# Kernel tuning notes

Hardware: AMD Instinct MI355X
Metric: run time of the kernel (lower is better)

The kernel has to match this reference:

```python
import jax, jax.numpy as jnp
import numpy as np

DIM = 64
HID = 128
DT_MAX = 0.1
BATCH = 16384


def _lin_init(k, fi, fo):
    kw, kb = jax.random.split(k)
    s = 1.0 / np.sqrt(fi)
    w = jax.random.uniform(kw, (fi, fo), minval=-s, maxval=s, dtype=jnp.float32)
    b = jax.random.uniform(kb, (fo,), minval=-s, maxval=s, dtype=jnp.float32)
    return w, b


def setup_inputs() -> dict:
    key = jax.random.key(0)
    ks = list(jax.random.split(key, 16))
    it = iter(ks)
    inp = {"z": jax.random.normal(next(it), (BATCH, DIM), dtype=jnp.float32)}
    layouts = [
        ("H", [(DIM, HID), (HID, HID), (HID, 1)]),
        ("D", [(DIM, HID), (HID, HID), (HID, 1)]),
        ("J", [(DIM, HID), (HID, DIM * DIM)]),
        ("B", [(DIM, HID), (HID, DIM * DIM)]),
        ("u", [(DIM, HID), (HID, DIM)]),
    ]
    for name, dims in layouts:
        for li, (fi, fo) in enumerate(dims, 1):
            w, b = _lin_init(next(it), fi, fo)
            inp[f"{name}w{li}"] = w
            inp[f"{name}b{li}"] = b
    inp["dt_logit"] = jnp.zeros((), dtype=jnp.float32)
    inp["energy_target"] = jnp.asarray(1.0, dtype=jnp.float32)
    return inp


def _scalar_net(z, w1, b1, w2, b2, w3, b3):
    # Linear->SiLU->Linear->SiLU->Linear, then softplus, squeeze -> [B]
    h = jax.nn.silu(z @ w1 + b1)
    h = jax.nn.silu(h @ w2 + b2)
    return jax.nn.softplus((h @ w3 + b3)[..., 0])


def reference(z, Hw1, Hb1, Hw2, Hb2, Hw3, Hb3,
              Dw1, Db1, Dw2, Db2, Dw3, Db3,
              Jw1, Jb1, Jw2, Jb2, Bw1, Bb1, Bw2, Bb2,
              uw1, ub1, uw2, ub2, dt_logit, energy_target):
    H = _scalar_net(z, Hw1, Hb1, Hw2, Hb2, Hw3, Hb3)  # [B]
    # autograd.grad(H.sum(), z) / grad(D.sum(), z)
    gH = jax.grad(lambda zz: _scalar_net(zz, Hw1, Hb1, Hw2, Hb2, Hw3, Hb3).sum())(z)
    gD = jax.grad(lambda zz: _scalar_net(zz, Dw1, Db1, Dw2, Db2, Dw3, Db3).sum())(z)
    # skew-symmetric J
    A = (jax.nn.silu(z @ Jw1 + Jb1) @ Jw2 + Jb2).reshape(-1, DIM, DIM)
    Jm = A - jnp.swapaxes(A, 1, 2)
    # PSD R = B B^T
    Bm = (jax.nn.silu(z @ Bw1 + Bb1) @ Bw2 + Bb2).reshape(-1, DIM, DIM)
    R = jnp.einsum('bik,bjk->bij', Bm, Bm)
    cons = jnp.einsum('bij,bj->bi', Jm, gH)
    diss = -jnp.einsum('bij,bj->bi', R, gD)
    u = jnp.tanh(z @ uw1 + ub1) @ uw2 + ub2
    pump = (energy_target - H)[:, None] * u
    dt = jax.nn.sigmoid(dt_logit) * DT_MAX
    dz = cons + diss + 0.1 * pump
    return z + dt * dz
```

## Files before the change

kernel.cpp:

```cpp
#include <hip/hip_runtime.h>

#define DIM 64
#define HID 128

typedef __attribute__((ext_vector_type(8))) short short8;
typedef __attribute__((ext_vector_type(4))) float f32x4;
typedef __attribute__((ext_vector_type(2))) float f32x2;
typedef _Float16 h16x8 __attribute__((ext_vector_type(8)));
typedef _Float16 h16x2 __attribute__((ext_vector_type(2)));
typedef unsigned short ushort_t;

#define MFMA(A, B, C) __builtin_amdgcn_mfma_f32_16x16x32_bf16((A), (B), (C), 0, 0, 0)
#define MFMAH(A, B, C) __builtin_amdgcn_mfma_f32_16x16x32_f16((A), (B), (C), 0, 0, 0)
#define GLOAD_LDS(gp, lp) __builtin_amdgcn_global_load_lds( \
    (const __attribute__((address_space(1))) void*)(gp),    \
    (__attribute__((address_space(3))) void*)(lp), 16, 0, 0)

__device__ __forceinline__ float sigm(float x) { return 1.f / (1.f + __expf(-x)); }
__device__ __forceinline__ float siluf(float x) { return x * sigm(x); }
__device__ __forceinline__ float silup(float x) { float s = sigm(x); return s + x * s * (1.f - s); }
__device__ __forceinline__ float softplusf(float x) {
    if (x > 20.f) return x;
    return log1pf(__expf(x));
}
__device__ __forceinline__ ushort_t f2bf(float f) {
    union { float f; unsigned int u; } v; v.f = f;
    unsigned int r = v.u + 0x7fffu + ((v.u >> 16) & 1u);
    return (ushort_t)(r >> 16);
}
__device__ __forceinline__ ushort_t f2h(float f) {
    _Float16 h = (_Float16)f;
    union { _Float16 h; ushort_t u; } v; v.h = h; return v.u;
}
__device__ __forceinline__ _Float16 u2h(ushort_t u) {
    union { ushort_t u; _Float16 h; } v; v.u = u; return v.h;
}

#define OFF_HW1F  0
#define OFF_HW2F  8192
#define OFF_HW2TF 24576
#define OFF_HW1TF 40960
#define OFF_DW1F  49152
#define OFF_DW2F  57344
#define OFF_DW2TF 73728
#define OFF_DW1TF 90112
#define OFF_UW1F  98304
#define OFF_UW2F  106496
#define OFF_JW1F  114688
#define OFF_BW1F  122880

extern "C" __global__ __launch_bounds__(256)
void prep3_kernel(const float* __restrict__ Jw2, const float* __restrict__ Jb2,
                  const float* __restrict__ Bw2, const float* __restrict__ Bb2,
                  const float* __restrict__ Hw1, const float* __restrict__ Hw2,
                  const float* __restrict__ Dw1, const float* __restrict__ Dw2,
                  const float* __restrict__ uw1, const float* __restrict__ uw2,
                  const float* __restrict__ Jw1, const float* __restrict__ Bw1,
                  ushort_t* __restrict__ JW, ushort_t* __restrict__ BW1, ushort_t* __restrict__ BW2,
                  ushort_t* __restrict__ JbdF, ushort_t* __restrict__ Bb2F, ushort_t* __restrict__ Bb2TF,
                  ushort_t* __restrict__ SWF)
{
    const int b = blockIdx.x;
    if (b < 6144) {
        const int m = b >> 11;
        const int o = ((b & 2047) << 8) | threadIdx.x;
        const int e = o & 7, n = (o >> 3) & 63, g = (o >> 9) & 3, kt = o >> 11;
        const int k = (kt << 5) | (g << 3) | e;
        const int oi = k >> 7, h = k & 127;
        float val;
        if (m == 0)      val = Jw2[h * 4096 + n * 64 + oi] - Jw2[h * 4096 + oi * 64 + n];
        else if (m == 1) val = Bw2[h * 4096 + oi * 64 + n];
        else             val = Bw2[h * 4096 + n * 64 + oi];
        ushort_t* dst = (m == 0) ? JW : (m == 1) ? BW1 : BW2;
        dst[o] = f2h(val);
    } else if (b == 6144) {
        for (int e0 = threadIdx.x; e0 < 12288; e0 += 256) {
            const int m = e0 >> 12, o = e0 & 4095;
            const int e = o & 7, n = (o >> 3) & 63, g = (o >> 9) & 3, kb = o >> 11;
            const int k = (kb << 5) | (g << 3) | e;
            float val; ushort_t* dst;
            if (m == 0)      { val = Jb2[n * 64 + k] - Jb2[k * 64 + n]; dst = JbdF; }
            else if (m == 1) { val = Bb2[k * 64 + n];                   dst = Bb2F; }
            else             { val = Bb2[n * 64 + k];                   dst = Bb2TF; }
            dst[o] = f2h(val);
        }
    } else {
        const int e = (b - 6145) * 256 + threadIdx.x;
        float val = 0.f;
        if (e < 98304) {
            const int net = e / 49152;
            const int o = e - net * 49152;
            const float* W1s = net ? Dw1 : Hw1;
            const float* W2s = net ? Dw2 : Hw2;
            if (o < 8192) {
                int ks = o & 31, n = (o >> 5) & 127, kt = o >> 12;
                val = W1s[(kt * 32 + ks) * 128 + n];
            } else if (o < 24576) {
                int o2 = o - 8192;
                int ks = o2 & 31, n = (o2 >> 5) & 127, kt = o2 >> 12;
                val = W2s[(kt * 32 + ks) * 128 + n];
            } else if (o < 40960) {
                int o3 = o - 24576;
                int ks = o3 & 31, n = (o3 >> 5) & 127, kt = o3 >> 12;
                val = W2s[n * 128 + kt * 32 + ks];
            } else {
                int o4 = o - 40960;
                int ks = o4 & 31, n = (o4 >> 5) & 63, kt = o4 >> 11;
                val = W1s[n * 128 + kt * 32 + ks];
            }
        } else if (e < 106496) {
            int o = e - 98304;
            int ks = o & 31, n = (o >> 5) & 127, kt = o >> 12;
            val = uw1[(kt * 32 + ks) * 128 + n];
        } else if (e < 114688) {
            int o = e - 106496;
            int ks = o & 31, n = (o >> 5) & 63, kt = o >> 11;
            val = uw2[(kt * 32 + ks) * 64 + n];
        } else if (e < 122880) {
            int o = e - 114688;
            int ks = o & 31, n = (o >> 5) & 127, kt = o >> 12;
            val = Jw1[(kt * 32 + ks) * 128 + n];
        } else {
            int o = e - 122880;
            int ks = o & 31, n = (o >> 5) & 127, kt = o >> 12;
            val = Bw1[(kt * 32 + ks) * 128 + n];
        }
        SWF[e] = f2bf(val);
    }
}

__device__ __forceinline__ void scalar_net(
    int tid, int r0,
    const ushort_t* zbp, ushort_t* S1, ushort_t* S2, ushort_t* S3,
    float* yacc, float* srow, float* Hrow,
    const ushort_t* W1f, const ushort_t* W2f, const ushort_t* W2Tf, const ushort_t* W1Tf,
    const float* B1, const float* B2, const float* W3, const float* B3,
    ushort_t* gOut, int storeH)
{
    const int lane = tid & 63, w = tid >> 6;
    const int mt = w & 3, nh = w >> 2;
    const int cl = lane & 15, qq = lane >> 4;
    const int arow = mt * 16 + cl;
    const int crow = mt * 16 + qq * 4;

    {
        short8 a0 = *(const short8*)&zbp[arow * 72 + (qq << 3)];
        short8 a1 = *(const short8*)&zbp[arow * 72 + 32 + (qq << 3)];
        #pragma unroll
        for (int nt = 0; nt < 4; ++nt) {
            int n = nh * 64 + nt * 16 + cl;
            f32x4 acc = {0.f, 0.f, 0.f, 0.f};
            short8 b0 = *(const short8*)&W1f[(n << 5) + (qq << 3)];
            short8 b1 = *(const short8*)&W1f[((128 + n) << 5) + (qq << 3)];
            acc = MFMA(a0, b0, acc); acc = MFMA(a1, b1, acc);
            float bv = B1[n];
            #pragma unroll
            for (int q = 0; q < 4; ++q) {
                float aa = acc[q] + bv;
                S1[(crow + q) * 136 + n] = f2bf(siluf(aa));
                S2[(crow + q) * 136 + n] = f2bf(silup(aa));
            }
        }
    }
    __syncthreads();
    {
        short8 a[4];
        #pragma unroll
        for (int kt = 0; kt < 4; ++kt)
            a[kt] = *(const short8*)&S1[arow * 136 + kt * 32 + (qq << 3)];
        float yp[4] = {0.f, 0.f, 0.f, 0.f};
        #pragma unroll
        for (int nt = 0; nt < 4; ++nt) {
            int n = nh * 64 + nt * 16 + cl;
            f32x4 acc = {0.f, 0.f, 0.f, 0.f};
            #pragma unroll
            for (int kt = 0; kt < 4; ++kt) {
                short8 bb = *(const short8*)&W2f[((kt * 128 + n) << 5) + (qq << 3)];
                acc = MFMA(a[kt], bb, acc);
            }
            float bv = B2[n], w3v = W3[n];
            #pragma unroll
            for (int q = 0; q < 4; ++q) {
                float a2 = acc[q] + bv;
                yp[q] += siluf(a2) * w3v;
                S3[(crow + q) * 136 + n] = f2bf(w3v * silup(a2));
            }
        }
        #pragma unroll
        for (int q = 0; q < 4; ++q) {
            float p = yp[q];
            p += __shfl_xor(p, 1); p += __shfl_xor(p, 2);
            p += __shfl_xor(p, 4); p += __shfl_xor(p, 8);
            if (cl == 0) atomicAdd(&yacc[crow + q], p);
        }
    }
    __syncthreads();
    if (tid < 64) {
        float a3 = yacc[tid] + B3[0];
        srow[tid] = sigm(a3);
        if (storeH) Hrow[tid] = softplusf(a3);
        yacc[tid] = 0.f;
    }
    __syncthreads();
    {
        short8 a[4];
        #pragma unroll
        for (int kt = 0; kt < 4; ++kt)
            a[kt] = *(const short8*)&S3[arow * 136 + kt * 32 + (qq << 3)];
        #pragma unroll
        for (int nt = 0; nt < 4; ++nt) {
            int n = nh * 64 + nt * 16 + cl;
            f32x4 acc = {0.f, 0.f, 0.f, 0.f};
            #pragma unroll
            for (int kt = 0; kt < 4; ++kt) {
                short8 bb = *(const short8*)&W2Tf[((kt * 128 + n) << 5) + (qq << 3)];
                acc = MFMA(a[kt], bb, acc);
            }
            #pragma unroll
            for (int q = 0; q < 4; ++q) {
                float sp;
                { union { unsigned int u; float f; } v;
                  v.u = ((unsigned int)S2[(crow + q) * 136 + n]) << 16; sp = v.f; }
                S1[(crow + q) * 136 + n] = f2bf(acc[q] * sp);
            }
        }
    }
    __syncthreads();
    {
        short8 a[4];
        #pragma unroll
        for (int kt = 0; kt < 4; ++kt)
            a[kt] = *(const short8*)&S1[arow * 136 + kt * 32 + (qq << 3)];
        #pragma unroll
        for (int ntl = 0; ntl < 2; ++ntl) {
            int n = nh * 32 + ntl * 16 + cl;
            f32x4 acc = {0.f, 0.f, 0.f, 0.f};
            #pragma unroll
            for (int kt = 0; kt < 4; ++kt) {
                short8 bb = *(const short8*)&W1Tf[((kt * 64 + n) << 5) + (qq << 3)];
                acc = MFMA(a[kt], bb, acc);
            }
            #pragma unroll
            for (int q = 0; q < 4; ++q) {
                int row = crow + q;
                gOut[(size_t)(r0 + row) * 64 + n] = f2h(srow[row] * acc[q]);
            }
        }
    }
    __syncthreads();
}

extern "C" __global__ __launch_bounds__(512, 4)
void k1_kernel(const float* __restrict__ z,
               const float* __restrict__ Hb1, const float* __restrict__ Hb2,
               const float* __restrict__ Hw3, const float* __restrict__ Hb3,
               const float* __restrict__ Db1, const float* __restrict__ Db2,
               const float* __restrict__ Dw3, const float* __restrict__ Db3,
               const float* __restrict__ ub1, const float* __restrict__ ub2,
               const float* __restrict__ dtl, const float* __restrict__ etg,
               const ushort_t* __restrict__ SWF,
               ushort_t* __restrict__ gHbf, ushort_t* __restrict__ gDbf,
               float* __restrict__ out)
{
    __shared__ __align__(16) ushort_t zb[64][72];
    __shared__ __align__(16) ushort_t S1[64][136];
    __shared__ __align__(16) ushort_t S2[64][136];
    __shared__ __align__(16) ushort_t S3[64][136];
    __shared__ float yacc[64];
    __shared__ float srow[64];
    __shared__ float Hrow[64];

    const int tid = threadIdx.x;
    const int r0 = blockIdx.x * 64;

    {
        const float4* zg = (const float4*)(z + (size_t)r0 * 64);
        #pragma unroll
        for (int it = 0; it < 2; ++it) {
            int i = it * 512 + tid;
            float4 v = zg[i];
            int row = i >> 4, c4 = (i & 15) * 4;
            zb[row][c4 + 0] = f2bf(v.x); zb[row][c4 + 1] = f2bf(v.y);
            zb[row][c4 + 2] = f2bf(v.z); zb[row][c4 + 3] = f2bf(v.w);
        }
        if (tid < 64) yacc[tid] = 0.f;
    }
    __syncthreads();

    scalar_net(tid, r0, &zb[0][0], &S1[0][0], &S2[0][0], &S3[0][0], yacc, srow, Hrow,
               SWF + OFF_HW1F, SWF + OFF_HW2F, SWF + OFF_HW2TF, SWF + OFF_HW1TF,
               Hb1, Hb2, Hw3, Hb3, gHbf, 1);
    scalar_net(tid, r0, &zb[0][0], &S1[0][0], &S2[0][0], &S3[0][0], yacc, srow, Hrow,
               SWF + OFF_DW1F, SWF + OFF_DW2F, SWF + OFF_DW2TF, SWF + OFF_DW1TF,
               Db1, Db2, Dw3, Db3, gDbf, 0);

    const int lane = tid & 63, w = tid >> 6;
    const int mt = w & 3, nh = w >> 2;
    const int cl = lane & 15, qq = lane >> 4;
    const int arow = mt * 16 + cl;
    const int crow = mt * 16 + qq * 4;

    {
        short8 a0 = *(const short8*)&zb[arow][(qq << 3)];
        short8 a1 = *(const short8*)&zb[arow][32 + (qq << 3)];
        const ushort_t* W1f = SWF + OFF_UW1F;
        #pragma unroll
        for (int nt = 0; nt < 4; ++nt) {
            int n = nh * 64 + nt * 16 + cl;
            f32x4 acc = {0.f, 0.f, 0.f, 0.f};
            short8 b0 = *(const short8*)&W1f[(n << 5) + (qq << 3)];
            short8 b1 = *(const short8*)&W1f[((128 + n) << 5) + (qq << 3)];
            acc = MFMA(a0, b0, acc); acc = MFMA(a1, b1, acc);
            float bv = ub1[n];
            #pragma unroll
            for (int q = 0; q < 4; ++q)
                S1[crow + q][n] = f2bf(tanhf(acc[q] + bv));
        }
    }
    __syncthreads();
    {
        short8 a[4];
        #pragma unroll
        for (int kt = 0; kt < 4; ++kt)
            a[kt] = *(const short8*)&S1[arow][kt * 32 + (qq << 3)];
        const ushort_t* W2f = SWF + OFF_UW2F;
        const float dtv = 0.1f * sigm(dtl[0]);
        const float et = etg[0];
        #pragma unroll
        for (int ntl = 0; ntl < 2; ++ntl) {
            int n = nh * 32 + ntl * 16 + cl;
            f32x4 acc = {0.f, 0.f, 0.f, 0.f};
            #pragma unroll
            for (int kt = 0; kt < 4; ++kt) {
                short8 bb = *(const short8*)&W2f[((kt * 64 + n) << 5) + (qq << 3)];
                acc = MFMA(a[kt], bb, acc);
            }
            float bv = ub2[n];
            #pragma unroll
            for (int q = 0; q < 4; ++q) {
                int row = crow + q;
                size_t idx = (size_t)(r0 + row) * 64 + n;
                out[idx] = z[idx] + dtv * 0.1f * (et - Hrow[row]) * (acc[q] + bv);
            }
        }
    }
}

#define LOADHF2H(SRC, HA, HB)                                                     \
    do {                                                                          \
        _Pragma("unroll")                                                         \
        for (int q4 = 0; q4 < 4; ++q4) {                                          \
            short8 sa = *(const short8*)&(SRC)[rr0][q4 * 32 + (qq << 3)];         \
            short8 sb = *(const short8*)&(SRC)[rr1][q4 * 32 + (qq << 3)];         \
            _Pragma("unroll")                                                     \
            for (int e = 0; e < 4; ++e) {                                         \
                h16x2 ta, tb;                                                     \
                ta[0] = u2h((ushort_t)sa[e * 2]); ta[1] = u2h((ushort_t)sa[e * 2 + 1]); \
                tb[0] = u2h((ushort_t)sb[e * 2]); tb[1] = u2h((ushort_t)sb[e * 2 + 1]); \
                (HA)[q4 * 4 + e] = ta;                                            \
                (HB)[q4 * 4 + e] = tb;                                            \
            }                                                                     \
        }                                                                         \
    } while (0)

#define STAGE(dst, src)                                                           \
    do {                                                                          \
        _Pragma("unroll")                                                         \
        for (int i_ = 0; i_ < 4; ++i_) {                                          \
            GLOAD_LDS((src) + ((w * 4 + i_) << 9) + (lane << 3),                  \
                      (dst) + ((w * 4 + i_) << 9));                               \
        }                                                                         \
    } while (0)

#define HEAVY_PASS(Wbase, BFbase, G, HA, HB, A00, A01, A10, A11)                  \
    do {                                                                          \
        STAGE(wst0, (Wbase));                                                     \
        __syncthreads();                                                          \
        _Pragma("unroll 1")                                                       \
        for (int t = 0; t < 32; ++t) {                                            \
            const ushort_t* curb = (t & 1) ? wst1 : wst0;                         \
            if (t < 31) STAGE((t & 1) ? wst0 : wst1, (Wbase) + (size_t)(t + 1) * 16384); \
            const int j = 2 * t + ks;                                             \
            _Float16 gA = u2h((G)[rr0][j]);                                       \
            _Float16 gB = u2h((G)[rr1][j]);                                       \
            h16x2 gA2; gA2[0] = gA; gA2[1] = gA;                                  \
            h16x2 gB2; gB2[0] = gB; gB2[1] = gB;                                  \
            _Pragma("unroll")                                                     \
            for (int ki = 0; ki < 4; ++ki) {                                      \
                const int tb = ((ks * 4 + ki) << 11) + (qq << 9);                 \
                h16x8 b0 = *(const h16x8*)&curb[tb + col0 * 8];                   \
                h16x8 b1 = *(const h16x8*)&curb[tb + col1 * 8];                   \
                union { h16x2 h2[4]; h16x8 v; } aA, aB;                           \
                _Pragma("unroll")                                                 \
                for (int e = 0; e < 4; ++e) {                                     \
                    aA.h2[e] = (HA)[ki * 4 + e] * gA2;                            \
                    aB.h2[e] = (HB)[ki * 4 + e] * gB2;                            \
                }                                                                 \
                A00 = MFMAH(aA.v, b0, A00); A01 = MFMAH(aA.v, b1, A01);           \
                A10 = MFMAH(aB.v, b0, A10); A11 = MFMAH(aB.v, b1, A11);           \
            }                                                                     \
            __syncthreads();                                                      \
        }                                                                         \
                        \
        {                                                                         \
            h16x8 abA = *(const h16x8*)&(G)[rr0][(ks << 5) + (qq << 3)];          \
            h16x8 abB = *(const h16x8*)&(G)[rr1][(ks << 5) + (qq << 3)];          \
            const ushort_t* bp = (BFbase) + (ks << 11) + (qq << 9);               \
            h16x8 b0 = *(const h16x8*)&bp[col0 * 8];                              \
            h16x8 b1 = *(const h16x8*)&bp[col1 * 8];                              \
            A00 = MFMAH(abA, b0, A00); A01 = MFMAH(abA, b1, A01);                 \
            A10 = MFMAH(abB, b0, A10); A11 = MFMAH(abB, b1, A11);                 \
        }                                                                         \
                                             \
        __syncthreads();                                                          \
        if (ks == 1) {                                                            \
            _Pragma("unroll")                                                     \
            for (int q = 0; q < 4; ++q) {                                         \
                Pb[orow0 + q][col0] = A00[q]; Pb[orow0 + q][col1] = A01[q];       \
                Pb[orow1 + q][col0] = A10[q]; Pb[orow1 + q][col1] = A11[q];       \
            }                                                                     \
        }                                                                         \
        __syncthreads();                                                          \
        if (ks == 0) {                                                            \
            _Pragma("unroll")                                                     \
            for (int q = 0; q < 4; ++q) {                                         \
                A00[q] += Pb[orow0 + q][col0]; A01[q] += Pb[orow0 + q][col1];     \
                A10[q] += Pb[orow1 + q][col0]; A11[q] += Pb[orow1 + q][col1];     \
            }                                                                     \
        }                                                                         \
        __syncthreads();                                                          \
    } while (0)

extern "C" __global__ __launch_bounds__(512, 2)
void k2_kernel(const float* __restrict__ z,
               const float* __restrict__ Jb1, const float* __restrict__ Bb1,
               const float* __restrict__ dtl,
               const ushort_t* __restrict__ JW, const ushort_t* __restrict__ BW1,
               const ushort_t* __restrict__ BW2,
               const ushort_t* __restrict__ JbdF, const ushort_t* __restrict__ Bb2F,
               const ushort_t* __restrict__ Bb2TF,
               const ushort_t* __restrict__ SWF,
               const ushort_t* __restrict__ gHbf, const ushort_t* __restrict__ gDbf,
               float* __restrict__ out)
{
    __shared__ __align__(16) ushort_t zb[64][72];
    __shared__ __align__(16) ushort_t hJ2[64][136];
    __shared__ __align__(16) ushort_t hB2[64][136];
    __shared__ __align__(16) ushort_t gHb[64][72];
    __shared__ __align__(16) ushort_t gDb[64][72];
    __shared__ __align__(16) ushort_t vb2[64][72];
    __shared__ __align__(16) float Pb[64][68];
    __shared__ __align__(16) ushort_t wst0[16384];
    __shared__ __align__(16) ushort_t wst1[16384];

    const int tid = threadIdx.x;
    const int r0 = blockIdx.x * 64;

    {
        const float4* zg = (const float4*)(z + (size_t)r0 * 64);
        #pragma unroll
        for (int it = 0; it < 2; ++it) {
            int i = it * 512 + tid;
            float4 v = zg[i];
            int row = i >> 4, c4 = (i & 15) * 4;
            zb[row][c4 + 0] = f2bf(v.x); zb[row][c4 + 1] = f2bf(v.y);
            zb[row][c4 + 2] = f2bf(v.z); zb[row][c4 + 3] = f2bf(v.w);
        }
        const short8* gh = (const short8*)(gHbf + (size_t)r0 * 64);
        const short8* gd = (const short8*)(gDbf + (size_t)r0 * 64);
        int row = tid >> 3, s = tid & 7;
        *(short8*)&gHb[row][s * 8] = gh[tid];
        *(short8*)&gDb[row][s * 8] = gd[tid];
    }
    __syncthreads();

    const int lane = tid & 63, w = tid >> 6;
    const int cl = lane & 15, qq = lane >> 4;
    const int mt = w & 3, nh = w >> 2;
    const int arow = mt * 16 + cl;
    const int crowL = mt * 16 + qq * 4;

    {
        short8 a0 = *(const short8*)&zb[arow][(qq << 3)];
        short8 a1 = *(const short8*)&zb[arow][32 + (qq << 3)];
        const ushort_t* JW1f = SWF + OFF_JW1F;
        const ushort_t* BW1f = SWF + OFF_BW1F;
        #pragma unroll
        for (int nt = 0; nt < 4; ++nt) {
            int n = nh * 64 + nt * 16 + cl;
            f32x4 accJ = {0.f, 0.f, 0.f, 0.f}, accB = {0.f, 0.f, 0.f, 0.f};
            short8 jb0 = *(const short8*)&JW1f[(n << 5) + (qq << 3)];
            short8 jb1 = *(const short8*)&JW1f[((128 + n) << 5) + (qq << 3)];
            accJ = MFMA(a0, jb0, accJ); accJ = MFMA(a1, jb1, accJ);
            short8 bb0 = *(const short8*)&BW1f[(n << 5) + (qq << 3)];
            short8 bb1 = *(const short8*)&BW1f[((128 + n) << 5) + (qq << 3)];
            accB = MFMA(a0, bb0, accB); accB = MFMA(a1, bb1, accB);
            float jbv = Jb1[n], bbv = Bb1[n];
            #pragma unroll
            for (int q = 0; q < 4; ++q) {
                hJ2[crowL + q][n] = f2h(siluf(accJ[q] + jbv));
                hB2[crowL + q][n] = f2h(siluf(accB[q] + bbv));
            }
        }
    }
    __syncthreads();

    const int ch = w & 1;
    const int ks = (w >> 1) & 1;
    const int rp = w >> 2;
    const int rr0 = rp * 32 + cl;
    const int rr1 = rr0 + 16;
    const int col0 = ch * 32 + cl;
    const int col1 = col0 + 16;
    const int orow0 = rp * 32 + qq * 4;
    const int orow1 = orow0 + 16;

    h16x2 hfJA[16], hfJB[16], hfBA[16], hfBB[16];
    f32x4 c00 = {0,0,0,0}, c01 = {0,0,0,0}, c10 = {0,0,0,0}, c11 = {0,0,0,0};
    f32x4 v00 = {0,0,0,0}, v01 = {0,0,0,0}, v10 = {0,0,0,0}, v11 = {0,0,0,0};
    f32x4 d00 = {0,0,0,0}, d01 = {0,0,0,0}, d10 = {0,0,0,0}, d11 = {0,0,0,0};

    LOADHF2H(hJ2, hfJA, hfJB);
    HEAVY_PASS(JW, JbdF, gHb, hfJA, hfJB, c00, c01, c10, c11);

    LOADHF2H(hB2, hfBA, hfBB);
    HEAVY_PASS(BW1, Bb2F, gDb, hfBA, hfBB, v00, v01, v10, v11);

    if (ks == 0) {
        #pragma unroll
        for (int q = 0; q < 4; ++q) {
            vb2[orow0 + q][col0] = f2h(v00[q]); vb2[orow0 + q][col1] = f2h(v01[q]);
            vb2[orow1 + q][col0] = f2h(v10[q]); vb2[orow1 + q][col1] = f2h(v11[q]);
        }
    }
    __syncthreads();

    HEAVY_PASS(BW2, Bb2TF, vb2, hfBA, hfBB, d00, d01, d10, d11);

    if (ks == 0) {
        const float dtv = 0.1f * sigm(dtl[0]);
        #pragma unroll
        for (int q = 0; q < 4; ++q) {
            size_t i00 = (size_t)(r0 + orow0 + q) * 64 + col0;
            size_t i01 = (size_t)(r0 + orow0 + q) * 64 + col1;
            size_t i10 = (size_t)(r0 + orow1 + q) * 64 + col0;
            size_t i11 = (size_t)(r0 + orow1 + q) * 64 + col1;
            out[i00] += dtv * (c00[q] - d00[q]);
            out[i01] += dtv * (c01[q] - d01[q]);
            out[i10] += dtv * (c10[q] - d10[q]);
            out[i11] += dtv * (c11[q] - d11[q]);
        }
    }
}

extern "C" void kernel_launch(void* const* d_in, const int* in_sizes, int n_in,
                              void* d_out, int out_size, void* d_ws, size_t ws_size,
                              hipStream_t stream) {
    const float* p[27];
    for (int i = 0; i < 27; ++i) p[i] = (const float*)d_in[i];
    ushort_t* JW    = (ushort_t*)d_ws;
    ushort_t* BW1   = JW + 524288;
    ushort_t* BW2   = BW1 + 524288;
    ushort_t* JbdF  = BW2 + 524288;
    ushort_t* Bb2F  = JbdF + 4096;
    ushort_t* Bb2TF = Bb2F + 4096;
    ushort_t* gHbf  = Bb2TF + 4096;
    ushort_t* gDbf  = gHbf + (size_t)16384 * 64;
    ushort_t* SWF   = gDbf + (size_t)16384 * 64;

    hipLaunchKernelGGL(prep3_kernel, dim3(6657), dim3(256), 0, stream,
                       p[15], p[16], p[19], p[20],
                       p[1], p[3], p[7], p[9],
                       p[21], p[23], p[13], p[17],
                       JW, BW1, BW2, JbdF, Bb2F, Bb2TF, SWF);

    const int batch = in_sizes[0] / DIM;
    hipLaunchKernelGGL(k1_kernel, dim3(batch / 64), dim3(512), 0, stream,
                       p[0],
                       p[2], p[4], p[5], p[6],
                       p[8], p[10], p[11], p[12],
                       p[22], p[24],
                       p[25], p[26],
                       SWF, gHbf, gDbf, (float*)d_out);

    hipLaunchKernelGGL(k2_kernel, dim3(batch / 64), dim3(512), 0, stream,
                       p[0], p[14], p[18], p[25],
                       JW, BW1, BW2, JbdF, Bb2F, Bb2TF, SWF,
                       gHbf, gDbf, (float*)d_out);
}
```

Before: 132.4 us.

## Halve k1 row tile to 32 and regroup k2 heavy-pass warps by column

```diff
diff --git a/kernel.cpp b/kernel.cpp
--- a/kernel.cpp
+++ b/kernel.cpp
@@ -5,7 +5,6 @@
 
 typedef __attribute__((ext_vector_type(8))) short short8;
 typedef __attribute__((ext_vector_type(4))) float f32x4;
-typedef __attribute__((ext_vector_type(2))) float f32x2;
 typedef _Float16 h16x8 __attribute__((ext_vector_type(8)));
 typedef _Float16 h16x2 __attribute__((ext_vector_type(2)));
 typedef unsigned short ushort_t;
@@ -138,7 +137,7 @@
     ushort_t* gOut, int storeH)
 {
     const int lane = tid & 63, w = tid >> 6;
-    const int mt = w & 3, nh = w >> 2;
+    const int mt = w & 1, nh = w >> 1;
     const int cl = lane & 15, qq = lane >> 4;
     const int arow = mt * 16 + cl;
     const int crow = mt * 16 + qq * 4;
@@ -147,8 +146,8 @@
         short8 a0 = *(const short8*)&zbp[arow * 72 + (qq << 3)];
         short8 a1 = *(const short8*)&zbp[arow * 72 + 32 + (qq << 3)];
         #pragma unroll
-        for (int nt = 0; nt < 4; ++nt) {
-            int n = nh * 64 + nt * 16 + cl;
+        for (int nt = 0; nt < 2; ++nt) {
+            int n = nh * 32 + nt * 16 + cl;
             f32x4 acc = {0.f, 0.f, 0.f, 0.f};
             short8 b0 = *(const short8*)&W1f[(n << 5) + (qq << 3)];
             short8 b1 = *(const short8*)&W1f[((128 + n) << 5) + (qq << 3)];
@@ -170,8 +169,8 @@
             a[kt] = *(const short8*)&S1[arow * 136 + kt * 32 + (qq << 3)];
         float yp[4] = {0.f, 0.f, 0.f, 0.f};
         #pragma unroll
-        for (int nt = 0; nt < 4; ++nt) {
-            int n = nh * 64 + nt * 16 + cl;
+        for (int nt = 0; nt < 2; ++nt) {
+            int n = nh * 32 + nt * 16 + cl;
             f32x4 acc = {0.f, 0.f, 0.f, 0.f};
             #pragma unroll
             for (int kt = 0; kt < 4; ++kt) {
@@ -195,7 +194,7 @@
         }
     }
     __syncthreads();
-    if (tid < 64) {
+    if (tid < 32) {
         float a3 = yacc[tid] + B3[0];
         srow[tid] = sigm(a3);
         if (storeH) Hrow[tid] = softplusf(a3);
@@ -208,8 +207,8 @@
         for (int kt = 0; kt < 4; ++kt)
             a[kt] = *(const short8*)&S3[arow * 136 + kt * 32 + (qq << 3)];
         #pragma unroll
-        for (int nt = 0; nt < 4; ++nt) {
-            int n = nh * 64 + nt * 16 + cl;
+        for (int nt = 0; nt < 2; ++nt) {
+            int n = nh * 32 + nt * 16 + cl;
             f32x4 acc = {0.f, 0.f, 0.f, 0.f};
             #pragma unroll
             for (int kt = 0; kt < 4; ++kt) {
@@ -231,20 +230,17 @@
         #pragma unroll
         for (int kt = 0; kt < 4; ++kt)
             a[kt] = *(const short8*)&S1[arow * 136 + kt * 32 + (qq << 3)];
-        #pragma unroll
-        for (int ntl = 0; ntl < 2; ++ntl) {
-            int n = nh * 32 + ntl * 16 + cl;
-            f32x4 acc = {0.f, 0.f, 0.f, 0.f};
-            #pragma unroll
-            for (int kt = 0; kt < 4; ++kt) {
-                short8 bb = *(const short8*)&W1Tf[((kt * 64 + n) << 5) + (qq << 3)];
-                acc = MFMA(a[kt], bb, acc);
-            }
-            #pragma unroll
-            for (int q = 0; q < 4; ++q) {
-                int row = crow + q;
-                gOut[(size_t)(r0 + row) * 64 + n] = f2h(srow[row] * acc[q]);
-            }
+        int n = nh * 16 + cl;
+        f32x4 acc = {0.f, 0.f, 0.f, 0.f};
+        #pragma unroll
+        for (int kt = 0; kt < 4; ++kt) {
+            short8 bb = *(const short8*)&W1Tf[((kt * 64 + n) << 5) + (qq << 3)];
+            acc = MFMA(a[kt], bb, acc);
+        }
+        #pragma unroll
+        for (int q = 0; q < 4; ++q) {
+            int row = crow + q;
+            gOut[(size_t)(r0 + row) * 64 + n] = f2h(srow[row] * acc[q]);
         }
     }
     __syncthreads();
@@ -262,28 +258,24 @@
                ushort_t* __restrict__ gHbf, ushort_t* __restrict__ gDbf,
                float* __restrict__ out)
 {
-    __shared__ __align__(16) ushort_t zb[64][72];
-    __shared__ __align__(16) ushort_t S1[64][136];
-    __shared__ __align__(16) ushort_t S2[64][136];
-    __shared__ __align__(16) ushort_t S3[64][136];
-    __shared__ float yacc[64];
-    __shared__ float srow[64];
-    __shared__ float Hrow[64];
+    __shared__ __align__(16) ushort_t zb[32][72];
+    __shared__ __align__(16) ushort_t S1[32][136];
+    __shared__ __align__(16) ushort_t S2[32][136];
+    __shared__ __align__(16) ushort_t S3[32][136];
+    __shared__ float yacc[32];
+    __shared__ float srow[32];
+    __shared__ float Hrow[32];
 
     const int tid = threadIdx.x;
-    const int r0 = blockIdx.x * 64;
+    const int r0 = blockIdx.x * 32;
 
     {
         const float4* zg = (const float4*)(z + (size_t)r0 * 64);
-        #pragma unroll
-        for (int it = 0; it < 2; ++it) {
-            int i = it * 512 + tid;
-            float4 v = zg[i];
-            int row = i >> 4, c4 = (i & 15) * 4;
-            zb[row][c4 + 0] = f2bf(v.x); zb[row][c4 + 1] = f2bf(v.y);
-            zb[row][c4 + 2] = f2bf(v.z); zb[row][c4 + 3] = f2bf(v.w);
-        }
-        if (tid < 64) yacc[tid] = 0.f;
+        float4 v = zg[tid];
+        int row = tid >> 4, c4 = (tid & 15) * 4;
+        zb[row][c4 + 0] = f2bf(v.x); zb[row][c4 + 1] = f2bf(v.y);
+        zb[row][c4 + 2] = f2bf(v.z); zb[row][c4 + 3] = f2bf(v.w);
+        if (tid < 32) yacc[tid] = 0.f;
     }
     __syncthreads();
 
@@ -295,7 +287,7 @@
                Db1, Db2, Dw3, Db3, gDbf, 0);
 
     const int lane = tid & 63, w = tid >> 6;
-    const int mt = w & 3, nh = w >> 2;
+    const int mt = w & 1, nh = w >> 1;
     const int cl = lane & 15, qq = lane >> 4;
     const int arow = mt * 16 + cl;
     const int crow = mt * 16 + qq * 4;
@@ -305,8 +297,8 @@
         short8 a1 = *(const short8*)&zb[arow][32 + (qq << 3)];
         const ushort_t* W1f = SWF + OFF_UW1F;
         #pragma unroll
-        for (int nt = 0; nt < 4; ++nt) {
-            int n = nh * 64 + nt * 16 + cl;
+        for (int nt = 0; nt < 2; ++nt) {
+            int n = nh * 32 + nt * 16 + cl;
             f32x4 acc = {0.f, 0.f, 0.f, 0.f};
             short8 b0 = *(const short8*)&W1f[(n << 5) + (qq << 3)];
             short8 b1 = *(const short8*)&W1f[((128 + n) << 5) + (qq << 3)];
@@ -326,39 +318,37 @@
         const ushort_t* W2f = SWF + OFF_UW2F;
         const float dtv = 0.1f * sigm(dtl[0]);
         const float et = etg[0];
-        #pragma unroll
-        for (int ntl = 0; ntl < 2; ++ntl) {
-            int n = nh * 32 + ntl * 16 + cl;
-            f32x4 acc = {0.f, 0.f, 0.f, 0.f};
-            #pragma unroll
-            for (int kt = 0; kt < 4; ++kt) {
-                short8 bb = *(const short8*)&W2f[((kt * 64 + n) << 5) + (qq << 3)];
-                acc = MFMA(a[kt], bb, acc);
-            }
-            float bv = ub2[n];
-            #pragma unroll
-            for (int q = 0; q < 4; ++q) {
-                int row = crow + q;
-                size_t idx = (size_t)(r0 + row) * 64 + n;
-                out[idx] = z[idx] + dtv * 0.1f * (et - Hrow[row]) * (acc[q] + bv);
-            }
-        }
-    }
-}
-
-#define LOADHF2H(SRC, HA, HB)                                                     \
+        int n = nh * 16 + cl;
+        f32x4 acc = {0.f, 0.f, 0.f, 0.f};
+        #pragma unroll
+        for (int kt = 0; kt < 4; ++kt) {
+            short8 bb = *(const short8*)&W2f[((kt * 64 + n) << 5) + (qq << 3)];
+            acc = MFMA(a[kt], bb, acc);
+        }
+        float bv = ub2[n];
+        #pragma unroll
+        for (int q = 0; q < 4; ++q) {
+            int row = crow + q;
+            size_t idx = (size_t)(r0 + row) * 64 + n;
+            out[idx] = z[idx] + dtv * 0.1f * (et - Hrow[row]) * (acc[q] + bv);
+        }
+    }
+}
+
+#define LOADHF4(SRC, HF)                                                          \
     do {                                                                          \
         _Pragma("unroll")                                                         \
-        for (int q4 = 0; q4 < 4; ++q4) {                                          \
-            short8 sa = *(const short8*)&(SRC)[rr0][q4 * 32 + (qq << 3)];         \
-            short8 sb = *(const short8*)&(SRC)[rr1][q4 * 32 + (qq << 3)];         \
+        for (int rt = 0; rt < 4; ++rt) {                                          \
             _Pragma("unroll")                                                     \
-            for (int e = 0; e < 4; ++e) {                                         \
-                h16x2 ta, tb;                                                     \
-                ta[0] = u2h((ushort_t)sa[e * 2]); ta[1] = u2h((ushort_t)sa[e * 2 + 1]); \
-                tb[0] = u2h((ushort_t)sb[e * 2]); tb[1] = u2h((ushort_t)sb[e * 2 + 1]); \
-                (HA)[q4 * 4 + e] = ta;                                            \
-                (HB)[q4 * 4 + e] = tb;                                            \
+            for (int q4 = 0; q4 < 4; ++q4) {                                      \
+                short8 s8 = *(const short8*)&(SRC)[rt * 16 + cl][q4 * 32 + (qq << 3)]; \
+                _Pragma("unroll")                                                 \
+                for (int e = 0; e < 4; ++e) {                                     \
+                    h16x2 t;                                                      \
+                    t[0] = u2h((ushort_t)s8[e * 2]);                              \
+                    t[1] = u2h((ushort_t)s8[e * 2 + 1]);                          \
+                    (HF)[rt][q4 * 4 + e] = t;                                     \
+                }                                                                 \
             }                                                                     \
         }                                                                         \
     } while (0)
@@ -372,7 +362,7 @@
         }                                                                         \
     } while (0)
 
-#define HEAVY_PASS(Wbase, BFbase, G, HA, HB, A00, A01, A10, A11)                  \
+#define HEAVY_PASS(Wbase, BFbase, G, HF, ACC)                                     \
     do {                                                                          \
         STAGE(wst0, (Wbase));                                                     \
         __syncthreads();                                                          \
@@ -381,52 +371,51 @@
             const ushort_t* curb = (t & 1) ? wst1 : wst0;                         \
             if (t < 31) STAGE((t & 1) ? wst0 : wst1, (Wbase) + (size_t)(t + 1) * 16384); \
             const int j = 2 * t + ks;                                             \
-            _Float16 gA = u2h((G)[rr0][j]);                                       \
-            _Float16 gB = u2h((G)[rr1][j]);                                       \
-            h16x2 gA2; gA2[0] = gA; gA2[1] = gA;                                  \
-            h16x2 gB2; gB2[0] = gB; gB2[1] = gB;                                  \
+            h16x2 g2[4];                                                          \
+            _Pragma("unroll")                                                     \
+            for (int rt = 0; rt < 4; ++rt) {                                      \
+                _Float16 gv = u2h((G)[rt * 16 + cl][j]);                          \
+                g2[rt][0] = gv; g2[rt][1] = gv;                                   \
+            }                                                                     \
             _Pragma("unroll")                                                     \
             for (int ki = 0; ki < 4; ++ki) {                                      \
-                const int tb = ((ks * 4 + ki) << 11) + (qq << 9);                 \
-                h16x8 b0 = *(const h16x8*)&curb[tb + col0 * 8];                   \
-                h16x8 b1 = *(const h16x8*)&curb[tb + col1 * 8];                   \
-                union { h16x2 h2[4]; h16x8 v; } aA, aB;                           \
+                h16x8 b = *(const h16x8*)&curb[((ks * 4 + ki) << 11) + (qq << 9) + col * 8]; \
                 _Pragma("unroll")                                                 \
-                for (int e = 0; e < 4; ++e) {                                     \
-                    aA.h2[e] = (HA)[ki * 4 + e] * gA2;                            \
-                    aB.h2[e] = (HB)[ki * 4 + e] * gB2;                            \
+                for (int rt = 0; rt < 4; ++rt) {                                  \
+                    union { h16x2 h2[4]; h16x8 v; } a;                            \
+                    _Pragma("unroll")                                             \
+                    for (int e = 0; e < 4; ++e)                                   \
+                        a.h2[e] = (HF)[rt][ki * 4 + e] * g2[rt];                  \
+                    ACC[rt] = MFMAH(a.v, b, ACC[rt]);                             \
                 }                                                                 \
-                A00 = MFMAH(aA.v, b0, A00); A01 = MFMAH(aA.v, b1, A01);           \
-                A10 = MFMAH(aB.v, b0, A10); A11 = MFMAH(aB.v, b1, A11);           \
             }                                                                     \
             __syncthreads();                                                      \
         }                                                                         \
-                        \
+                                    \
         {                                                                         \
-            h16x8 abA = *(const h16x8*)&(G)[rr0][(ks << 5) + (qq << 3)];          \
-            h16x8 abB = *(const h16x8*)&(G)[rr1][(ks << 5) + (qq << 3)];          \
-            const ushort_t* bp = (BFbase) + (ks << 11) + (qq << 9);               \
-            h16x8 b0 = *(const h16x8*)&bp[col0 * 8];                              \
-            h16x8 b1 = *(const h16x8*)&bp[col1 * 8];                              \
-            A00 = MFMAH(abA, b0, A00); A01 = MFMAH(abA, b1, A01);                 \
-            A10 = MFMAH(abB, b0, A10); A11 = MFMAH(abB, b1, A11);                 \
+            h16x8 b = *(const h16x8*)((BFbase) + (ks << 11) + (qq << 9) + col * 8); \
+            _Pragma("unroll")                                                     \
+            for (int rt = 0; rt < 4; ++rt) {                                      \
+                h16x8 ab = *(const h16x8*)&(G)[rt * 16 + cl][(ks << 5) + (qq << 3)]; \
+                ACC[rt] = MFMAH(ab, b, ACC[rt]);                                  \
+            }                                                                     \
         }                                                                         \
                                              \
         __syncthreads();                                                          \
         if (ks == 1) {                                                            \
             _Pragma("unroll")                                                     \
-            for (int q = 0; q < 4; ++q) {                                         \
-                Pb[orow0 + q][col0] = A00[q]; Pb[orow0 + q][col1] = A01[q];       \
-                Pb[orow1 + q][col0] = A10[q]; Pb[orow1 + q][col1] = A11[q];       \
-            }                                                                     \
+            for (int rt = 0; rt < 4; ++rt)                                        \
+                _Pragma("unroll")                                                 \
+                for (int q = 0; q < 4; ++q)                                       \
+                    Pb[rt * 16 + qq * 4 + q][col] = ACC[rt][q];                   \
         }                                                                         \
         __syncthreads();                                                          \
         if (ks == 0) {                                                            \
             _Pragma("unroll")                                                     \
-            for (int q = 0; q < 4; ++q) {                                         \
-                A00[q] += Pb[orow0 + q][col0]; A01[q] += Pb[orow0 + q][col1];     \
-                A10[q] += Pb[orow1 + q][col0]; A11[q] += Pb[orow1 + q][col1];     \
-            }                                                                     \
+            for (int rt = 0; rt < 4; ++rt)                                        \
+                _Pragma("unroll")                                                 \
+                for (int q = 0; q < 4; ++q)                                       \
+                    ACC[rt][q] += Pb[rt * 16 + qq * 4 + q][col];                  \
         }                                                                         \
         __syncthreads();                                                          \
     } while (0)
@@ -505,51 +494,45 @@
     }
     __syncthreads();
 
-    const int ch = w & 1;
-    const int ks = (w >> 1) & 1;
-    const int rp = w >> 2;
-    const int rr0 = rp * 32 + cl;
-    const int rr1 = rr0 + 16;
-    const int col0 = ch * 32 + cl;
-    const int col1 = col0 + 16;
-    const int orow0 = rp * 32 + qq * 4;
-    const int orow1 = orow0 + 16;
-
-    h16x2 hfJA[16], hfJB[16], hfBA[16], hfBB[16];
-    f32x4 c00 = {0,0,0,0}, c01 = {0,0,0,0}, c10 = {0,0,0,0}, c11 = {0,0,0,0};
-    f32x4 v00 = {0,0,0,0}, v01 = {0,0,0,0}, v10 = {0,0,0,0}, v11 = {0,0,0,0};
-    f32x4 d00 = {0,0,0,0}, d01 = {0,0,0,0}, d10 = {0,0,0,0}, d11 = {0,0,0,0};
-
-    LOADHF2H(hJ2, hfJA, hfJB);
-    HEAVY_PASS(JW, JbdF, gHb, hfJA, hfJB, c00, c01, c10, c11);
-
-    LOADHF2H(hB2, hfBA, hfBB);
-    HEAVY_PASS(BW1, Bb2F, gDb, hfBA, hfBB, v00, v01, v10, v11);
+    const int cq = w & 3;
+    const int ks = w >> 2;
+    const int col = cq * 16 + cl;
+
+    h16x2 hf[4][16];
+    f32x4 cA[4], vA[4], dA[4];
+    #pragma unroll
+    for (int rt = 0; rt < 4; ++rt) {
+        cA[rt] = (f32x4){0.f, 0.f, 0.f, 0.f};
+        vA[rt] = (f32x4){0.f, 0.f, 0.f, 0.f};
+        dA[rt] = (f32x4){0.f, 0.f, 0.f, 0.f};
+    }
+
+    LOADHF4(hJ2, hf);
+    HEAVY_PASS(JW, JbdF, gHb, hf, cA);
+
+    LOADHF4(hB2, hf);
+    HEAVY_PASS(BW1, Bb2F, gDb, hf, vA);
 
     if (ks == 0) {
         #pragma unroll
-        for (int q = 0; q < 4; ++q) {
-            vb2[orow0 + q][col0] = f2h(v00[q]); vb2[orow0 + q][col1] = f2h(v01[q]);
-            vb2[orow1 + q][col0] = f2h(v10[q]); vb2[orow1 + q][col1] = f2h(v11[q]);
-        }
-    }
-    __syncthreads();
-
-    HEAVY_PASS(BW2, Bb2TF, vb2, hfBA, hfBB, d00, d01, d10, d11);
+        for (int rt = 0; rt < 4; ++rt)
+            #pragma unroll
+            for (int q = 0; q < 4; ++q)
+                vb2[rt * 16 + qq * 4 + q][col] = f2h(vA[rt][q]);
+    }
+    __syncthreads();
+
+    HEAVY_PASS(BW2, Bb2TF, vb2, hf, dA);
 
     if (ks == 0) {
         const float dtv = 0.1f * sigm(dtl[0]);
         #pragma unroll
-        for (int q = 0; q < 4; ++q) {
-            size_t i00 = (size_t)(r0 + orow0 + q) * 64 + col0;
-            size_t i01 = (size_t)(r0 + orow0 + q) * 64 + col1;
-            size_t i10 = (size_t)(r0 + orow1 + q) * 64 + col0;
-            size_t i11 = (size_t)(r0 + orow1 + q) * 64 + col1;
-            out[i00] += dtv * (c00[q] - d00[q]);
-            out[i01] += dtv * (c01[q] - d01[q]);
-            out[i10] += dtv * (c10[q] - d10[q]);
-            out[i11] += dtv * (c11[q] - d11[q]);
-        }
+        for (int rt = 0; rt < 4; ++rt)
+            #pragma unroll
+            for (int q = 0; q < 4; ++q) {
+                size_t idx = (size_t)(r0 + rt * 16 + qq * 4 + q) * 64 + col;
+                out[idx] += dtv * (cA[rt][q] - dA[rt][q]);
+            }
     }
 }
 
@@ -575,7 +558,7 @@
                        JW, BW1, BW2, JbdF, Bb2F, Bb2TF, SWF);
 
     const int batch = in_sizes[0] / DIM;
-    hipLaunchKernelGGL(k1_kernel, dim3(batch / 64), dim3(512), 0, stream,
+    hipLaunchKernelGGL(k1_kernel, dim3(batch / 32), dim3(512), 0, stream,
                        p[0],
                        p[2], p[4], p[5], p[6],
                        p[8], p[10], p[11], p[12],
```

Measured after the change: 127.4 us. -3.8%, faster.
